# Optimization experiments

Hardware: AMD Instinct MI355X
Metric: run time of the kernel (lower is better)

Reference implementation:

```python
import jax, jax.numpy as jnp
import numpy as np

N_NODES = 50000
N_EVENTS = 500000
P = 127          # previous_embed_size
A = P + 1        # agg_features
O = A + P        # w2 out size = 255
BN_EPS = 1e-5


def setup_inputs() -> dict:
    key = jax.random.key(0)
    ks = jax.random.split(key, 12)
    inp = {
        "u": jax.random.randint(ks[0], (N_EVENTS,), 0, N_NODES),
        "v": jax.random.randint(ks[1], (N_EVENTS,), 0, N_NODES),
        "g": jax.random.uniform(ks[2], (N_EVENTS, 1), dtype=jnp.float32),
        "h": jax.random.normal(ks[3], (N_NODES, P), dtype=jnp.float32),
        "remember_u": jax.random.normal(ks[4], (N_EVENTS, P), dtype=jnp.float32),
        "remember_v": jax.random.normal(ks[5], (N_EVENTS, P), dtype=jnp.float32),
        "bn_gamma": jnp.ones((A,), jnp.float32),
        "bn_beta": jnp.zeros((A,), jnp.float32),
        "w1_w": jax.random.normal(ks[6], (A, A), dtype=jnp.float32) / np.sqrt(A),
        "w1_b": jax.random.normal(ks[7], (A,), dtype=jnp.float32) * 0.01,
        "w2_w": jax.random.normal(ks[8], (O, O), dtype=jnp.float32) / np.sqrt(O),
        "w2_b": jax.random.normal(ks[9], (O,), dtype=jnp.float32) * 0.01,
        "event": N_EVENTS,
    }
    return inp


def reference(u, v, g, h, remember_u, remember_v, bn_gamma, bn_beta,
              w1_w, w1_b, w2_w, w2_b, event):
    n_nodes = h.shape[0]
    agg_feat = bn_gamma.shape[0]
    # per-edge messages: cat(stale embedding, time feature)  -> [E, A]
    src_u = jnp.concatenate([remember_u, g], axis=1)
    src_v = jnp.concatenate([remember_v, g], axis=1)
    # scatter_add into node buffers (row-wise scatter, index expanded in torch)
    agg_v = jnp.zeros((n_nodes, agg_feat), g.dtype).at[v].add(src_u)
    agg_u = jnp.zeros((n_nodes, agg_feat), g.dtype).at[u].add(src_v)
    agg = agg_u + agg_v  # [N, A]
    # BatchNorm1d (training mode: batch stats over node dim, biased var)
    mean = jnp.mean(agg, axis=0)
    var = jnp.var(agg, axis=0)
    x = (agg - mean) * jax.lax.rsqrt(var + BN_EPS) * bn_gamma + bn_beta
    # 2-layer MLP with skip-cat of h
    x1 = jax.nn.relu(x @ w1_w.T + w1_b)                 # [N, A]
    out = jnp.concatenate([h, x1], axis=1) @ w2_w.T + w2_b  # [N, A+P]
    return out
```

## Files before the change

kernel.cpp:

```cpp
#include <hip/hip_runtime.h>

constexpr int PDIM = 127;
constexpr int ADIM = 128;
constexpr int ODIM = 255;
constexpr int RTILE = 16;
constexpr int CAP = 80;
constexpr float EPS = 1e-5f;

constexpr int XS_STRIDE = 136;
constexpr int CS_STRIDE = 264;

typedef short bf16x8 __attribute__((ext_vector_type(8)));
typedef float f32x4 __attribute__((ext_vector_type(4)));

__device__ inline unsigned short f2b(float x) {
    unsigned u = __builtin_bit_cast(unsigned, x);
    u += 0x7FFF + ((u >> 16) & 1);
    return (unsigned short)(u >> 16);
}

__global__ __launch_bounds__(256) void bucket_kernel(
    const int* __restrict__ u, const int* __restrict__ v,
    int* __restrict__ cnt, int* __restrict__ bucket, int E)
{
    int e = blockIdx.x * 256 + threadIdx.x;
    if (e >= E) return;
    int vn = v[e];
    int slot = atomicAdd(&cnt[vn], 1);
    if (slot < CAP) bucket[(long long)vn * CAP + slot] = e;
    int un = u[e];
    slot = atomicAdd(&cnt[un], 1);
    if (slot < CAP) bucket[(long long)un * CAP + slot] = e | (1 << 20);
}

__global__ __launch_bounds__(256) void gather_kernel(
    const int* __restrict__ cnt, const int* __restrict__ bucket,
    const float* __restrict__ g,
    const float* __restrict__ ru, const float* __restrict__ rv,
    float* __restrict__ agg, int N)
{
    int wid0 = (blockIdx.x * 256 + threadIdx.x) >> 6;
    if (wid0 >= N) return;
    int wid = __builtin_amdgcn_readfirstlane(wid0);
    int lane = threadIdx.x & 63;
    int deg = cnt[wid];
    if (deg > CAP) deg = CAP;
    const int* bkt = bucket + (long long)wid * CAP;
    int j = lane * 2;
    bool full = (j + 1 < PDIM);
    int j1 = full ? j + 1 : PDIM - 1;
    float a0 = 0.f, a1 = 0.f;
    int d = 0;
    for (; d + 4 <= deg; d += 4) {
        int c0 = bkt[d + 0], c1 = bkt[d + 1], c2 = bkt[d + 2], c3 = bkt[d + 3];
        int e0 = c0 & 0xFFFFF, e1 = c1 & 0xFFFFF, e2 = c2 & 0xFFFFF, e3 = c3 & 0xFFFFF;
        const float* s0 = (c0 & (1 << 20)) ? rv : ru;
        const float* s1 = (c1 & (1 << 20)) ? rv : ru;
        const float* s2 = (c2 & (1 << 20)) ? rv : ru;
        const float* s3 = (c3 & (1 << 20)) ? rv : ru;
        long long B0 = (long long)e0 * PDIM, B1 = (long long)e1 * PDIM;
        long long B2 = (long long)e2 * PDIM, B3 = (long long)e3 * PDIM;
        float p0 = s0[B0 + j], q0 = full ? s0[B0 + j1] : g[e0];
        float p1 = s1[B1 + j], q1 = full ? s1[B1 + j1] : g[e1];
        float p2 = s2[B2 + j], q2 = full ? s2[B2 + j1] : g[e2];
        float p3 = s3[B3 + j], q3 = full ? s3[B3 + j1] : g[e3];
        a0 += p0 + p1 + p2 + p3;
        a1 += q0 + q1 + q2 + q3;
    }
    for (; d < deg; ++d) {
        int c = bkt[d];
        int e = c & 0xFFFFF;
        const float* s = (c & (1 << 20)) ? rv : ru;
        long long B = (long long)e * PDIM;
        a0 += s[B + j];
        a1 += full ? s[B + j1] : g[e];
    }
    float2 val; val.x = a0; val.y = a1;
    *reinterpret_cast<float2*>(&agg[(long long)wid * ADIM + j]) = val;
}

__global__ __launch_bounds__(256) void colstats_kernel(
    const float* __restrict__ agg, float* __restrict__ csum,
    float* __restrict__ csumsq, int N)
{
    int j = threadIdx.x & 127;
    int rh = threadIdx.x >> 7;
    float s = 0.f, ss = 0.f;
    for (int r = blockIdx.x * 2 + rh; r < N; r += gridDim.x * 2) {
        float x = agg[(long long)r * ADIM + j];
        s += x; ss += x * x;
    }
    __shared__ float sh[2][128];
    __shared__ float sh2[2][128];
    sh[rh][j] = s; sh2[rh][j] = ss;
    __syncthreads();
    if (threadIdx.x < 128) {
        unsafeAtomicAdd(&csum[j], sh[0][j] + sh[1][j]);
        unsafeAtomicAdd(&csumsq[j], sh2[0][j] + sh2[1][j]);
    }
}

__global__ void finalize_kernel(const float* __restrict__ csum,
                                const float* __restrict__ csumsq,
                                const float* __restrict__ gamma,
                                const float* __restrict__ beta,
                                float* __restrict__ scale,
                                float* __restrict__ shift, int N)
{
    int j = threadIdx.x;
    if (j >= ADIM) return;
    float inv = 1.f / (float)N;
    float mean = csum[j] * inv;
    float var = csumsq[j] * inv - mean * mean;
    float sc = gamma[j] * rsqrtf(var + EPS);
    scale[j] = sc;
    shift[j] = beta[j] - mean * sc;
}

__global__ __launch_bounds__(256) void wprep_kernel(
    const float* __restrict__ w1, const float* __restrict__ w2,
    unsigned short* __restrict__ w1b, unsigned short* __restrict__ w2b)
{
    int t = blockIdx.x * 256 + threadIdx.x;
    if (t < 65536) {
        int o = t >> 8, k = t & 255;
        w2b[t] = (o < ODIM && k < ODIM) ? f2b(w2[o * ODIM + k]) : (unsigned short)0;
    } else {
        int s = t - 65536;
        if (s < ADIM * ADIM) w1b[s] = f2b(w1[s]);
    }
}

__global__ __launch_bounds__(256) void mlp_kernel(
    const float* __restrict__ agg, const float* __restrict__ h,
    const float* __restrict__ scale, const float* __restrict__ shift,
    const unsigned short* __restrict__ w1b, const float* __restrict__ b1,
    const unsigned short* __restrict__ w2b, const float* __restrict__ b2,
    float* __restrict__ out, int N)
{
    __shared__ unsigned short xs[RTILE * XS_STRIDE];
    __shared__ unsigned short cs[RTILE * CS_STRIDE];
    int tid = threadIdx.x;
    int row0 = blockIdx.x * RTILE;
    int lane = tid & 63;
    int wave = tid >> 6;

    {
        int j = tid & 127, rh = tid >> 7;
        float sc = scale[j], sf = shift[j];
        for (int i = 0; i < 8; ++i) {
            int r = i * 2 + rh;
            long long grow = row0 + r;
            float x = agg[grow * ADIM + j] * sc + sf;
            xs[r * XS_STRIDE + j] = f2b(x);
            float hv = (j < PDIM) ? h[grow * PDIM + j] : 0.f;
            cs[r * CS_STRIDE + j] = f2b(hv);
        }
        if (tid < RTILE) cs[tid * CS_STRIDE + 255] = 0;
    }
    __syncthreads();

    {
        int arow = lane & 15, akg = lane >> 4;
        bf16x8 afr[4];
        #pragma unroll
        for (int ks = 0; ks < 4; ++ks)
            afr[ks] = *reinterpret_cast<const bf16x8*>(&xs[arow * XS_STRIDE + ks * 32 + akg * 8]);
        #pragma unroll
        for (int t = 0; t < 2; ++t) {
            int bcol = (wave * 2 + t) * 16 + (lane & 15);
            f32x4 acc = {0.f, 0.f, 0.f, 0.f};
            #pragma unroll
            for (int ks = 0; ks < 4; ++ks) {
                bf16x8 bfr = *reinterpret_cast<const bf16x8*>(&w1b[bcol * ADIM + ks * 32 + akg * 8]);
                acc = __builtin_amdgcn_mfma_f32_16x16x32_bf16(afr[ks], bfr, acc, 0, 0, 0);
            }
            float bias = b1[bcol];
            #pragma unroll
            for (int i = 0; i < 4; ++i) {
                int r = (lane >> 4) * 4 + i;
                float x1 = fmaxf(acc[i] + bias, 0.f);
                cs[r * CS_STRIDE + PDIM + bcol] = f2b(x1);
            }
        }
    }
    __syncthreads();

    {
        int arow = lane & 15, akg = lane >> 4;
        bf16x8 afr[8];
        #pragma unroll
        for (int ks = 0; ks < 8; ++ks)
            afr[ks] = *reinterpret_cast<const bf16x8*>(&cs[arow * CS_STRIDE + ks * 32 + akg * 8]);
        #pragma unroll
        for (int t = 0; t < 4; ++t) {
            int o = (wave * 4 + t) * 16 + (lane & 15);
            f32x4 acc = {0.f, 0.f, 0.f, 0.f};
            #pragma unroll
            for (int ks = 0; ks < 8; ++ks) {
                bf16x8 bfr = *reinterpret_cast<const bf16x8*>(&w2b[o * 256 + ks * 32 + akg * 8]);
                acc = __builtin_amdgcn_mfma_f32_16x16x32_bf16(afr[ks], bfr, acc, 0, 0, 0);
            }
            if (o < ODIM) {
                float bias = b2[o];
                #pragma unroll
                for (int i = 0; i < 4; ++i) {
                    long long grow = row0 + (lane >> 4) * 4 + i;
                    out[grow * ODIM + o] = acc[i] + bias;
                }
            }
        }
    }
}

extern "C" void kernel_launch(void* const* d_in, const int* in_sizes, int n_in,
                              void* d_out, int out_size, void* d_ws, size_t ws_size,
                              hipStream_t stream)
{
    const int*   u     = (const int*)d_in[0];
    const int*   v     = (const int*)d_in[1];
    const float* g     = (const float*)d_in[2];
    const float* h     = (const float*)d_in[3];
    const float* ru    = (const float*)d_in[4];
    const float* rv    = (const float*)d_in[5];
    const float* gamma = (const float*)d_in[6];
    const float* beta  = (const float*)d_in[7];
    const float* w1w   = (const float*)d_in[8];
    const float* w1b_f = (const float*)d_in[9];
    const float* w2w   = (const float*)d_in[10];
    const float* w2b_f = (const float*)d_in[11];

    int E = in_sizes[0];
    int N = in_sizes[3] / PDIM;

    int*   cnt    = (int*)d_ws;
    float* csum   = (float*)d_ws + N;
    float* csumsq = csum + ADIM;
    float* scale  = csumsq + ADIM;
    float* shift  = scale + ADIM;
    int*   bucket = (int*)(shift + ADIM);
    float* agg    = (float*)(bucket + (long long)N * CAP);
    unsigned short* w1b = (unsigned short*)(agg + (long long)N * ADIM);
    unsigned short* w2b = w1b + ADIM * ADIM;

    (void)hipMemsetAsync(cnt, 0, ((size_t)N + 2 * ADIM) * sizeof(float), stream);

    wprep_kernel<<<(65536 + ADIM * ADIM + 255) / 256, 256, 0, stream>>>(w1w, w2w, w1b, w2b);

    bucket_kernel<<<(E + 255) / 256, 256, 0, stream>>>(u, v, cnt, bucket, E);

    long long gthreads = (long long)N * 64;
    gather_kernel<<<(int)((gthreads + 255) / 256), 256, 0, stream>>>(
        cnt, bucket, g, ru, rv, agg, N);

    colstats_kernel<<<1024, 256, 0, stream>>>(agg, csum, csumsq, N);
    finalize_kernel<<<1, 128, 0, stream>>>(csum, csumsq, gamma, beta, scale, shift, N);

    int mblocks = (N + RTILE - 1) / RTILE;
    mlp_kernel<<<mblocks, 256, 0, stream>>>(agg, h, scale, shift, w1b, w1b_f, w2b, w2b_f,
                                            (float*)d_out, N);
}
```

Measured before the change: 324.5 us.

## Widen MLP row tile for weight reuse and make gather wave-coalesced

The MLP kernel now handles 32 rows per block instead of 16. Each weight fragment loaded from global memory feeds two MFMA row tiles, which halves weight traffic per row, and bounds checks allow N to be a partial tile. The gather kernel preloads each node's bucket indices into lanes and broadcasts them with readlane, so the index loads are no longer serialized. Each lane now reads contiguous columns, lane for the first half and 64+lane for the second (the last lane reads g), with 8 edges in flight per iteration. The trade-offs are more registers, fewer MLP blocks, and launch bounds that ask for 4 blocks per CU.

```diff
diff --git a/kernel.cpp b/kernel.cpp
--- a/kernel.cpp
+++ b/kernel.cpp
@@ -3,7 +3,7 @@
 constexpr int PDIM = 127;
 constexpr int ADIM = 128;
 constexpr int ODIM = 255;
-constexpr int RTILE = 16;
+constexpr int RTILE = 32;
 constexpr int CAP = 80;
 constexpr float EPS = 1e-5f;
 
@@ -46,37 +46,42 @@
     int deg = cnt[wid];
     if (deg > CAP) deg = CAP;
     const int* bkt = bucket + (long long)wid * CAP;
-    int j = lane * 2;
-    bool full = (j + 1 < PDIM);
-    int j1 = full ? j + 1 : PDIM - 1;
+    int cA = (lane < deg) ? bkt[lane] : 0;
+    int cB = (lane + 64 < deg) ? bkt[lane + 64] : 0;
+
     float a0 = 0.f, a1 = 0.f;
+    bool lo = (lane < 63);
+
     int d = 0;
-    for (; d + 4 <= deg; d += 4) {
-        int c0 = bkt[d + 0], c1 = bkt[d + 1], c2 = bkt[d + 2], c3 = bkt[d + 3];
-        int e0 = c0 & 0xFFFFF, e1 = c1 & 0xFFFFF, e2 = c2 & 0xFFFFF, e3 = c3 & 0xFFFFF;
-        const float* s0 = (c0 & (1 << 20)) ? rv : ru;
-        const float* s1 = (c1 & (1 << 20)) ? rv : ru;
-        const float* s2 = (c2 & (1 << 20)) ? rv : ru;
-        const float* s3 = (c3 & (1 << 20)) ? rv : ru;
-        long long B0 = (long long)e0 * PDIM, B1 = (long long)e1 * PDIM;
-        long long B2 = (long long)e2 * PDIM, B3 = (long long)e3 * PDIM;
-        float p0 = s0[B0 + j], q0 = full ? s0[B0 + j1] : g[e0];
-        float p1 = s1[B1 + j], q1 = full ? s1[B1 + j1] : g[e1];
-        float p2 = s2[B2 + j], q2 = full ? s2[B2 + j1] : g[e2];
-        float p3 = s3[B3 + j], q3 = full ? s3[B3 + j1] : g[e3];
-        a0 += p0 + p1 + p2 + p3;
-        a1 += q0 + q1 + q2 + q3;
+    for (; d + 8 <= deg; d += 8) {
+        float x0[8], x1[8];
+        #pragma unroll
+        for (int k = 0; k < 8; ++k) {
+            int dd = d + k;
+            int c = (dd < 64) ? __builtin_amdgcn_readlane(cA, dd)
+                              : __builtin_amdgcn_readlane(cB, dd - 64);
+            int e = c & 0xFFFFF;
+            const float* s = (c & (1 << 20)) ? rv : ru;
+            long long B = (long long)e * PDIM;
+            const float* p1 = lo ? (s + B + 64 + lane) : (g + e);
+            x0[k] = s[B + lane];
+            x1[k] = *p1;
+        }
+        #pragma unroll
+        for (int k = 0; k < 8; ++k) { a0 += x0[k]; a1 += x1[k]; }
     }
     for (; d < deg; ++d) {
-        int c = bkt[d];
+        int c = (d < 64) ? __builtin_amdgcn_readlane(cA, d)
+                         : __builtin_amdgcn_readlane(cB, d - 64);
         int e = c & 0xFFFFF;
         const float* s = (c & (1 << 20)) ? rv : ru;
         long long B = (long long)e * PDIM;
-        a0 += s[B + j];
-        a1 += full ? s[B + j1] : g[e];
-    }
-    float2 val; val.x = a0; val.y = a1;
-    *reinterpret_cast<float2*>(&agg[(long long)wid * ADIM + j]) = val;
+        const float* p1 = lo ? (s + B + 64 + lane) : (g + e);
+        a0 += s[B + lane];
+        a1 += *p1;
+    }
+    agg[(long long)wid * ADIM + lane] = a0;
+    agg[(long long)wid * ADIM + 64 + lane] = a1;
 }
 
 __global__ __launch_bounds__(256) void colstats_kernel(
@@ -131,7 +136,7 @@
     }
 }
 
-__global__ __launch_bounds__(256) void mlp_kernel(
+__global__ __launch_bounds__(256, 4) void mlp_kernel(
     const float* __restrict__ agg, const float* __restrict__ h,
     const float* __restrict__ scale, const float* __restrict__ shift,
     const unsigned short* __restrict__ w1b, const float* __restrict__ b1,
@@ -148,12 +153,15 @@
     {
         int j = tid & 127, rh = tid >> 7;
         float sc = scale[j], sf = shift[j];
-        for (int i = 0; i < 8; ++i) {
+        for (int i = 0; i < RTILE / 2; ++i) {
             int r = i * 2 + rh;
             long long grow = row0 + r;
-            float x = agg[grow * ADIM + j] * sc + sf;
+            float x = 0.f, hv = 0.f;
+            if (grow < N) {
+                x = agg[grow * ADIM + j] * sc + sf;
+                if (j < PDIM) hv = h[grow * PDIM + j];
+            }
             xs[r * XS_STRIDE + j] = f2b(x);
-            float hv = (j < PDIM) ? h[grow * PDIM + j] : 0.f;
             cs[r * CS_STRIDE + j] = f2b(hv);
         }
         if (tid < RTILE) cs[tid * CS_STRIDE + 255] = 0;
@@ -162,25 +170,33 @@
 
     {
         int arow = lane & 15, akg = lane >> 4;
-        bf16x8 afr[4];
-        #pragma unroll
-        for (int ks = 0; ks < 4; ++ks)
-            afr[ks] = *reinterpret_cast<const bf16x8*>(&xs[arow * XS_STRIDE + ks * 32 + akg * 8]);
+        bf16x8 afr[2][4];
+        #pragma unroll
+        for (int rt = 0; rt < 2; ++rt)
+            #pragma unroll
+            for (int ks = 0; ks < 4; ++ks)
+                afr[rt][ks] = *reinterpret_cast<const bf16x8*>(
+                    &xs[(rt * 16 + arow) * XS_STRIDE + ks * 32 + akg * 8]);
         #pragma unroll
         for (int t = 0; t < 2; ++t) {
             int bcol = (wave * 2 + t) * 16 + (lane & 15);
-            f32x4 acc = {0.f, 0.f, 0.f, 0.f};
-            #pragma unroll
-            for (int ks = 0; ks < 4; ++ks) {
-                bf16x8 bfr = *reinterpret_cast<const bf16x8*>(&w1b[bcol * ADIM + ks * 32 + akg * 8]);
-                acc = __builtin_amdgcn_mfma_f32_16x16x32_bf16(afr[ks], bfr, acc, 0, 0, 0);
-            }
+            bf16x8 bfr[4];
+            #pragma unroll
+            for (int ks = 0; ks < 4; ++ks)
+                bfr[ks] = *reinterpret_cast<const bf16x8*>(&w1b[bcol * ADIM + ks * 32 + akg * 8]);
             float bias = b1[bcol];
             #pragma unroll
-            for (int i = 0; i < 4; ++i) {
-                int r = (lane >> 4) * 4 + i;
-                float x1 = fmaxf(acc[i] + bias, 0.f);
-                cs[r * CS_STRIDE + PDIM + bcol] = f2b(x1);
+            for (int rt = 0; rt < 2; ++rt) {
+                f32x4 acc = {0.f, 0.f, 0.f, 0.f};
+                #pragma unroll
+                for (int ks = 0; ks < 4; ++ks)
+                    acc = __builtin_amdgcn_mfma_f32_16x16x32_bf16(afr[rt][ks], bfr[ks], acc, 0, 0, 0);
+                #pragma unroll
+                for (int i = 0; i < 4; ++i) {
+                    int r = rt * 16 + (lane >> 4) * 4 + i;
+                    float x1 = fmaxf(acc[i] + bias, 0.f);
+                    cs[r * CS_STRIDE + PDIM + bcol] = f2b(x1);
+                }
             }
         }
     }
@@ -188,25 +204,33 @@
 
     {
         int arow = lane & 15, akg = lane >> 4;
-        bf16x8 afr[8];
-        #pragma unroll
-        for (int ks = 0; ks < 8; ++ks)
-            afr[ks] = *reinterpret_cast<const bf16x8*>(&cs[arow * CS_STRIDE + ks * 32 + akg * 8]);
+        bf16x8 caf[2][8];
+        #pragma unroll
+        for (int rt = 0; rt < 2; ++rt)
+            #pragma unroll
+            for (int ks = 0; ks < 8; ++ks)
+                caf[rt][ks] = *reinterpret_cast<const bf16x8*>(
+                    &cs[(rt * 16 + arow) * CS_STRIDE + ks * 32 + akg * 8]);
         #pragma unroll
         for (int t = 0; t < 4; ++t) {
             int o = (wave * 4 + t) * 16 + (lane & 15);
-            f32x4 acc = {0.f, 0.f, 0.f, 0.f};
-            #pragma unroll
-            for (int ks = 0; ks < 8; ++ks) {
-                bf16x8 bfr = *reinterpret_cast<const bf16x8*>(&w2b[o * 256 + ks * 32 + akg * 8]);
-                acc = __builtin_amdgcn_mfma_f32_16x16x32_bf16(afr[ks], bfr, acc, 0, 0, 0);
-            }
-            if (o < ODIM) {
-                float bias = b2[o];
+            bf16x8 bfr[8];
+            #pragma unroll
+            for (int ks = 0; ks < 8; ++ks)
+                bfr[ks] = *reinterpret_cast<const bf16x8*>(&w2b[o * 256 + ks * 32 + akg * 8]);
+            float bias = (o < ODIM) ? b2[o] : 0.f;
+            #pragma unroll
+            for (int rt = 0; rt < 2; ++rt) {
+                f32x4 acc = {0.f, 0.f, 0.f, 0.f};
                 #pragma unroll
-                for (int i = 0; i < 4; ++i) {
-                    long long grow = row0 + (lane >> 4) * 4 + i;
-                    out[grow * ODIM + o] = acc[i] + bias;
+                for (int ks = 0; ks < 8; ++ks)
+                    acc = __builtin_amdgcn_mfma_f32_16x16x32_bf16(caf[rt][ks], bfr[ks], acc, 0, 0, 0);
+                if (o < ODIM) {
+                    #pragma unroll
+                    for (int i = 0; i < 4; ++i) {
+                        long long grow = row0 + rt * 16 + (lane >> 4) * 4 + i;
+                        if (grow < N) out[grow * ODIM + o] = acc[i] + bias;
+                    }
                 }
             }
         }
```

After: 304.1 us. -6.3%, faster.
